# Kernel optimization log

Measured on AMD Instinct MI355X. Metric: run time of the kernel, lower is better.

Reference implementation:

```python
import jax, jax.numpy as jnp
import numpy as np

N = 100000
E = 3200000
T = 8
F = 64


def _temporal_conv(x, src, dst, time_index, W, b):
    # time-bucketed segmented scatter-add: segment id = dst*T + t
    seg = dst * T + time_index                      # [E]
    msgs = x[src]                                   # [E, F] gather (x_j)
    agg = jax.ops.segment_sum(msgs, seg, num_segments=N * T)  # [N*T, F]
    cat = agg.reshape(N, T * x.shape[-1])           # concat over t blocks: [N, T*F]
    return jax.nn.relu(cat @ W + b)                 # temporal_lin + relu


def setup_inputs() -> dict:
    key = jax.random.key(0)
    ks = jax.random.split(key, 10)
    x = jax.random.normal(ks[0], (N, F), dtype=jnp.float32)
    edge_index = jax.random.randint(ks[1], (2, E), 0, N, dtype=jnp.int64)
    time_index = jax.random.randint(ks[2], (E,), 0, T, dtype=jnp.int64)
    s1 = 1.0 / np.sqrt(F * T)
    W1 = jax.random.uniform(ks[3], (F * T, 64), jnp.float32, -s1, s1)
    b1 = jax.random.uniform(ks[4], (64,), jnp.float32, -s1, s1)
    s2 = 1.0 / np.sqrt(64 * T)
    W2 = jax.random.uniform(ks[5], (64 * T, 64), jnp.float32, -s2, s2)
    b2 = jax.random.uniform(ks[6], (64,), jnp.float32, -s2, s2)
    s3 = 1.0 / np.sqrt(64)
    Wssl = jax.random.uniform(ks[7], (64, F), jnp.float32, -s3, s3)
    bssl = jax.random.uniform(ks[8], (F,), jnp.float32, -s3, s3)
    return {"x": x, "edge_index": edge_index, "time_index": time_index,
            "W1": W1, "b1": b1, "W2": W2, "b2": b2, "Wssl": Wssl, "bssl": bssl}


def reference(x, edge_index, time_index, W1, b1, W2, b2, Wssl, bssl):
    src, dst = edge_index[0], edge_index[1]  # flow source_to_target
    h = _temporal_conv(x, src, dst, time_index, W1, b1)
    h = jax.nn.relu(h)                        # outer relu in TemporalSSTGNN.forward
    h = _temporal_conv(h, src, dst, time_index, W2, b2)
    ssl = h @ Wssl + bssl                     # self_supervised_linear
    return (h, ssl)
```

## Files before the change

kernel.cpp:

```cpp
#include <hip/hip_runtime.h>
#include <hip/hip_bf16.h>

#define N_NODES 100000
#define N_EDGES 3200000
#define NB 391
#define NBP 400
#define CAP 9216
#define PCAP 20480
#define ZNODE N_NODES
#define AROW 520
#define HROW 72

typedef __attribute__((ext_vector_type(8))) short short8;
typedef __attribute__((ext_vector_type(4))) float floatx4;
typedef __attribute__((ext_vector_type(2))) float f32x2;

__device__ __forceinline__ unsigned short f2bf(float f) {
    unsigned int u = __builtin_bit_cast(unsigned int, f);
    unsigned int r = (u + 0x7FFFu + ((u >> 16) & 1u)) >> 16;
    return (unsigned short)r;
}

__global__ __launch_bounds__(1024) void k_bscatter(const int* __restrict__ ei,
                                                   const int* __restrict__ ti,
                                                   int* __restrict__ cursor,
                                                   unsigned int* __restrict__ words,
                                                   const float* __restrict__ x,
                                                   unsigned short* __restrict__ xb,
                                                   unsigned short* __restrict__ h1b,
                                                   const float* __restrict__ W1,
                                                   const float* __restrict__ W2,
                                                   const float* __restrict__ Wssl,
                                                   unsigned short* __restrict__ Wf1,
                                                   unsigned short* __restrict__ Wf2,
                                                   unsigned short* __restrict__ Wsf) {
    __shared__ int h[NBP];
    __shared__ int bb[NBP];
    int tid = threadIdx.x;
    if (tid < NBP) h[tid] = 0;
    __syncthreads();
    int base = blockIdx.x * 4096;
    int breg[4], ofs[4];
    unsigned wreg[4];
#pragma unroll
    for (int i = 0; i < 4; ++i) {
        int e = base + i * 1024 + tid;
        bool v = e < N_EDGES;
        int dst = v ? ei[N_EDGES + e] : 0;
        int src = v ? ei[e] : 0;
        int tt  = v ? ti[e] : 0;
        int b = dst >> 8;
        breg[i] = v ? b : -1;
        wreg[i] = ((unsigned)src << 11) | ((unsigned)(dst & 255) << 3) | (unsigned)tt;
        ofs[i] = v ? atomicAdd(&h[b], 1) : 0;
    }
    __syncthreads();
    if (tid < NB) {
        int c = h[tid];
        bb[tid] = c ? atomicAdd(&cursor[tid], c) : 0;
    }
    __syncthreads();
#pragma unroll
    for (int i = 0; i < 4; ++i)
        if (breg[i] >= 0) {
            int b = breg[i];
            words[b * CAP + bb[b] + ofs[i]] = wreg[i];
        }

    int gtid = blockIdx.x * 1024 + tid;
    size_t xo = (size_t)gtid * 8;
    if (xo < (size_t)N_NODES * 64) {
        float4 f0 = *(const float4*)(x + xo);
        float4 f1 = *(const float4*)(x + xo + 4);
        unsigned r0, r1, r2, r3;
        asm("v_cvt_pk_bf16_f32 %0, %1, %2" : "=v"(r0) : "v"(f0.x), "v"(f0.y));
        asm("v_cvt_pk_bf16_f32 %0, %1, %2" : "=v"(r1) : "v"(f0.z), "v"(f0.w));
        asm("v_cvt_pk_bf16_f32 %0, %1, %2" : "=v"(r2) : "v"(f1.x), "v"(f1.y));
        asm("v_cvt_pk_bf16_f32 %0, %1, %2" : "=v"(r3) : "v"(f1.z), "v"(f1.w));
        uint4 st; st.x = r0; st.y = r1; st.z = r2; st.w = r3;
        *(uint4*)(xb + xo) = st;
    }
    if (gtid < 64) {
        xb[(size_t)ZNODE * 64 + gtid] = 0;
        h1b[(size_t)ZNODE * 64 + gtid] = 0;
    }
    if (gtid < 512 * 64) {
        int k = gtid >> 6, o = gtid & 63;
        int c = o >> 4, m = o & 15;
        int ks = k >> 5, q = (k >> 3) & 3, j = k & 7;
        int pos = (((c * 16 + ks) * 64) + (m + 16 * q)) * 8 + j;
        Wf1[pos] = f2bf(W1[gtid]);
        Wf2[pos] = f2bf(W2[gtid]);
    }
    if (gtid < 64 * 64) {
        int k = gtid >> 6, o = gtid & 63;
        int c = o >> 4, m = o & 15;
        int ks = k >> 5, q = (k >> 3) & 3, j = k & 7;
        int pos = (((c * 2 + ks) * 64) + (m + 16 * q)) * 8 + j;
        Wsf[pos] = f2bf(Wssl[gtid]);
    }
}

__global__ __launch_bounds__(1024) void k_lsort(const int* __restrict__ cursor,
                                                const unsigned int* __restrict__ words,
                                                int2* __restrict__ node_pm,
                                                int* __restrict__ gid_pad) {
    __shared__ int h[2048];
    __shared__ int nb[256];
    __shared__ int s_ml[256];
    __shared__ int wsum[4];
    int tid = threadIdx.x;
    int b = blockIdx.x;
    int rb = b * CAP, re = rb + cursor[b];
    h[tid] = 0; h[tid + 1024] = 0;
    __syncthreads();
    unsigned wreg[9];
    int ofs[9];
#pragma unroll
    for (int i = 0; i < 9; ++i) {
        int e = rb + i * 1024 + tid;
        bool v = e < re;
        unsigned w = v ? words[e] : 0u;
        wreg[i] = w;
        ofs[i] = v ? atomicAdd(&h[w & 2047u], 1) : -1;
    }
    __syncthreads();
    int sz = 0;
    if (tid < 256) {
        int m = 0;
#pragma unroll
        for (int t = 0; t < 8; ++t) { int c = h[tid * 8 + t]; m = c > m ? c : m; }
        m = (m + 3) & ~3;
        if (m < 8) m = 8;
        s_ml[tid] = m;
        sz = m * 8;
    }
    int lane = tid & 63, wv = tid >> 6;
    int inc = sz;
#pragma unroll
    for (int off = 1; off < 64; off <<= 1) {
        int t = __shfl_up(inc, off, 64);
        if (lane >= off) inc += t;
    }
    if (tid < 256 && lane == 63) wsum[wv] = inc;
    __syncthreads();
    int bsz = wsum[0] + wsum[1] + wsum[2] + wsum[3];
    if (tid < 256) {
        int basec = 0;
        for (int w = 0; w < wv; ++w) basec += wsum[w];
        nb[tid] = basec + inc - sz;
    }
    int pbase = b * PCAP;
    for (int s = tid; s < bsz; s += 1024) gid_pad[pbase + s] = ZNODE;
    int gn = b * 256 + tid;
    if (tid < 256 && gn < N_NODES) node_pm[gn] = (int2){pbase + nb[tid], s_ml[tid]};
    __syncthreads();
#pragma unroll
    for (int i = 0; i < 9; ++i)
        if (ofs[i] >= 0) {
            unsigned w = wreg[i];
            int ls = (int)(w & 2047u);
            int nd = ls >> 3, t = ls & 7;
            gid_pad[pbase + nb[nd] + t * s_ml[nd] + ofs[i]] = (int)(w >> 11);
        }
}


__device__ __forceinline__ void accumP(f32x2* a, uint4 p) {
    uint2 u;
    u.x = p.x << 16; u.y = p.x & 0xFFFF0000u;
    a[0] += __builtin_bit_cast(f32x2, u);
    u.x = p.y << 16; u.y = p.y & 0xFFFF0000u;
    a[1] += __builtin_bit_cast(f32x2, u);
    u.x = p.z << 16; u.y = p.z & 0xFFFF0000u;
    a[2] += __builtin_bit_cast(f32x2, u);
    u.x = p.w << 16; u.y = p.w & 0xFFFF0000u;
    a[3] += __builtin_bit_cast(f32x2, u);
}

__global__ __launch_bounds__(512) void k_fused(const int2* __restrict__ node_pm,
                                               const int* __restrict__ gid_pad,
                                               const unsigned short* __restrict__ xb,
                                               const unsigned short* __restrict__ Wf,
                                               const float* __restrict__ bias,
                                               const unsigned short* __restrict__ Wsf,
                                               const float* __restrict__ bssl,
                                               unsigned short* __restrict__ out_bf,
                                               float* __restrict__ out_f32,
                                               float* __restrict__ ssl_out) {
    __shared__ __align__(16) unsigned short Atile[32 * AROW];
    int tid = threadIdx.x;
    int wave = tid >> 6, lane = tid & 63;
    int node_base = blockIdx.x * 32;
    int tl = lane >> 3, fo = lane & 7;
    const uint4* xs = (const uint4*)xb;

    int2 pm[4];
#pragma unroll
    for (int i = 0; i < 4; ++i) pm[i] = node_pm[node_base + wave * 4 + i];

    int pb[4], ml[4];
    const int* gp[4];
#pragma unroll
    for (int i = 0; i < 4; ++i) {
        pb[i] = __builtin_amdgcn_readfirstlane(pm[i].x);
        ml[i] = __builtin_amdgcn_readfirstlane(pm[i].y);
        gp[i] = gid_pad + pb[i] + tl * ml[i];
    }
    int4 ga[4], gb[4];
#pragma unroll
    for (int i = 0; i < 4; ++i) {
        ga[i] = *(const int4*)(gp[i]);
        gb[i] = *(const int4*)(gp[i] + 4);
    }

#pragma unroll
    for (int pr = 0; pr < 2; ++pr) {
        int i0 = pr * 2, i1 = i0 + 1;
        uint4 p0 = xs[((unsigned)ga[i0].x << 3) + fo];
        uint4 p1 = xs[((unsigned)ga[i0].y << 3) + fo];
        uint4 p2 = xs[((unsigned)ga[i0].z << 3) + fo];
        uint4 p3 = xs[((unsigned)ga[i0].w << 3) + fo];
        uint4 p4 = xs[((unsigned)gb[i0].x << 3) + fo];
        uint4 p5 = xs[((unsigned)gb[i0].y << 3) + fo];
        uint4 p6 = xs[((unsigned)gb[i0].z << 3) + fo];
        uint4 p7 = xs[((unsigned)gb[i0].w << 3) + fo];
        uint4 q0 = xs[((unsigned)ga[i1].x << 3) + fo];
        uint4 q1 = xs[((unsigned)ga[i1].y << 3) + fo];
        uint4 q2 = xs[((unsigned)ga[i1].z << 3) + fo];
        uint4 q3 = xs[((unsigned)ga[i1].w << 3) + fo];
        uint4 q4 = xs[((unsigned)gb[i1].x << 3) + fo];
        uint4 q5 = xs[((unsigned)gb[i1].y << 3) + fo];
        uint4 q6 = xs[((unsigned)gb[i1].z << 3) + fo];
        uint4 q7 = xs[((unsigned)gb[i1].w << 3) + fo];
        f32x2 a0[4] = {{0.f,0.f},{0.f,0.f},{0.f,0.f},{0.f,0.f}};
        f32x2 a1[4] = {{0.f,0.f},{0.f,0.f},{0.f,0.f},{0.f,0.f}};
        accumP(a0, p0); accumP(a0, p1); accumP(a0, p2); accumP(a0, p3);
        accumP(a0, p4); accumP(a0, p5); accumP(a0, p6); accumP(a0, p7);
        accumP(a1, q0); accumP(a1, q1); accumP(a1, q2); accumP(a1, q3);
        accumP(a1, q4); accumP(a1, q5); accumP(a1, q6); accumP(a1, q7);
#pragma unroll 1
        for (int k = 8; k < ml[i0]; k += 4) {
            int4 g = *(const int4*)(gp[i0] + k);
            uint4 t0 = xs[((unsigned)g.x << 3) + fo];
            uint4 t1 = xs[((unsigned)g.y << 3) + fo];
            uint4 t2 = xs[((unsigned)g.z << 3) + fo];
            uint4 t3 = xs[((unsigned)g.w << 3) + fo];
            accumP(a0, t0); accumP(a0, t1); accumP(a0, t2); accumP(a0, t3);
        }
#pragma unroll 1
        for (int k = 8; k < ml[i1]; k += 4) {
            int4 g = *(const int4*)(gp[i1] + k);
            uint4 t0 = xs[((unsigned)g.x << 3) + fo];
            uint4 t1 = xs[((unsigned)g.y << 3) + fo];
            uint4 t2 = xs[((unsigned)g.z << 3) + fo];
            uint4 t3 = xs[((unsigned)g.w << 3) + fo];
            accumP(a1, t0); accumP(a1, t1); accumP(a1, t2); accumP(a1, t3);
        }
        unsigned r0, r1, r2, r3;
        asm("v_cvt_pk_bf16_f32 %0, %1, %2" : "=v"(r0) : "v"(a0[0].x), "v"(a0[0].y));
        asm("v_cvt_pk_bf16_f32 %0, %1, %2" : "=v"(r1) : "v"(a0[1].x), "v"(a0[1].y));
        asm("v_cvt_pk_bf16_f32 %0, %1, %2" : "=v"(r2) : "v"(a0[2].x), "v"(a0[2].y));
        asm("v_cvt_pk_bf16_f32 %0, %1, %2" : "=v"(r3) : "v"(a0[3].x), "v"(a0[3].y));
        uint4 st; st.x = r0; st.y = r1; st.z = r2; st.w = r3;
        *(uint4*)(&Atile[(wave * 4 + i0) * AROW + tl * 64 + fo * 8]) = st;
        asm("v_cvt_pk_bf16_f32 %0, %1, %2" : "=v"(r0) : "v"(a1[0].x), "v"(a1[0].y));
        asm("v_cvt_pk_bf16_f32 %0, %1, %2" : "=v"(r1) : "v"(a1[1].x), "v"(a1[1].y));
        asm("v_cvt_pk_bf16_f32 %0, %1, %2" : "=v"(r2) : "v"(a1[2].x), "v"(a1[2].y));
        asm("v_cvt_pk_bf16_f32 %0, %1, %2" : "=v"(r3) : "v"(a1[3].x), "v"(a1[3].y));
        st.x = r0; st.y = r1; st.z = r2; st.w = r3;
        *(uint4*)(&Atile[(wave * 4 + i1) * AROW + tl * 64 + fo * 8]) = st;
    }
    __syncthreads();

    int nt = wave >> 2, c = wave & 3;
    int m = lane & 15, q = lane >> 4;
    floatx4 acc = (floatx4){0.f, 0.f, 0.f, 0.f};
    const short8* wf8 = (const short8*)Wf;
    const unsigned short* abase = &Atile[(nt * 16 + m) * AROW + q * 8];
#pragma unroll
    for (int ks = 0; ks < 16; ++ks) {
        short8 a = *(const short8*)(abase + ks * 32);
        short8 b = wf8[(c * 16 + ks) * 64 + lane];
        acc = __builtin_amdgcn_mfma_f32_16x16x32_bf16(a, b, acc, 0, 0, 0);
    }
    float bb = bias[c * 16 + m];
    int node0 = node_base + nt * 16;
    float vv[4];
#pragma unroll
    for (int i = 0; i < 4; ++i) {
        float v = acc[i] + bb;
        vv[i] = v > 0.f ? v : 0.f;
        int node = node0 + q * 4 + i;
        size_t idx = (size_t)node * 64 + c * 16 + m;
        if (out_bf)  out_bf[idx] = f2bf(vv[i]);
        if (out_f32) out_f32[idx] = vv[i];
    }

    if (ssl_out) {
        __syncthreads();
        unsigned short* Ht = Atile;
#pragma unroll
        for (int i = 0; i < 4; ++i) {
            int nl = nt * 16 + q * 4 + i;
            Ht[nl * HROW + c * 16 + m] = f2bf(vv[i]);
        }
        __syncthreads();
        int nt2 = wave >> 2, c2 = wave & 3;
        floatx4 sacc = (floatx4){0.f, 0.f, 0.f, 0.f};
        const short8* sw8 = (const short8*)Wsf;
        const unsigned short* sab = &Ht[(nt2 * 16 + m) * HROW + q * 8];
#pragma unroll
        for (int ks = 0; ks < 2; ++ks) {
            short8 a = *(const short8*)(sab + ks * 32);
            short8 b = sw8[(c2 * 2 + ks) * 64 + lane];
            sacc = __builtin_amdgcn_mfma_f32_16x16x32_bf16(a, b, sacc, 0, 0, 0);
        }
        float sb = bssl[c2 * 16 + m];
        int n0 = node_base + nt2 * 16;
#pragma unroll
        for (int i = 0; i < 4; ++i) {
            int node = n0 + q * 4 + i;
            ssl_out[(size_t)node * 64 + c2 * 16 + m] = sacc[i] + sb;
        }
    }
}


extern "C" void kernel_launch(void* const* d_in, const int* in_sizes, int n_in,
                              void* d_out, int out_size, void* d_ws, size_t ws_size,
                              hipStream_t stream) {
    const float* x    = (const float*)d_in[0];
    const int*   ei   = (const int*)d_in[1];
    const int*   ti   = (const int*)d_in[2];
    const float* W1   = (const float*)d_in[3];
    const float* b1   = (const float*)d_in[4];
    const float* W2   = (const float*)d_in[5];
    const float* b2   = (const float*)d_in[6];
    const float* Wssl = (const float*)d_in[7];
    const float* bssl = (const float*)d_in[8];
    float* out = (float*)d_out;

    char* w = (char*)d_ws;
    auto alloc = [&](size_t bytes) -> char* {
        char* p = w;
        w += (bytes + 255) & ~(size_t)255;
        return p;
    };
    int* cursor   = (int*)alloc((size_t)NBP * 4);
    unsigned int* words = (unsigned int*)alloc((size_t)NB * CAP * 4);
    int2* node_pm = (int2*)alloc((size_t)N_NODES * 8);
    int* gid_pad  = (int*)alloc((size_t)NB * PCAP * 4);
    unsigned short* xb  = (unsigned short*)alloc((size_t)(N_NODES + 1) * 64 * 2);
    unsigned short* h1b = (unsigned short*)alloc((size_t)(N_NODES + 1) * 64 * 2);
    unsigned short* Wf1 = (unsigned short*)alloc((size_t)512 * 64 * 2);
    unsigned short* Wf2 = (unsigned short*)alloc((size_t)512 * 64 * 2);
    unsigned short* Wsf = (unsigned short*)alloc((size_t)64 * 64 * 2);

    hipMemsetAsync(cursor, 0, (size_t)NBP * 4, stream);
    k_bscatter<<<(N_EDGES + 4095) / 4096, 1024, 0, stream>>>(ei, ti, cursor, words,
                                                             x, xb, h1b, W1, W2, Wssl,
                                                             Wf1, Wf2, Wsf);
    k_lsort<<<NB, 1024, 0, stream>>>(cursor, words, node_pm, gid_pad);

    k_fused<<<N_NODES / 32, 512, 0, stream>>>(node_pm, gid_pad, xb, Wf1, b1,
                                              nullptr, nullptr, h1b, nullptr, nullptr);
    k_fused<<<N_NODES / 32, 512, 0, stream>>>(node_pm, gid_pad, h1b, Wf2, b2,
                                              Wsf, bssl, nullptr, out,
                                              out + (size_t)N_NODES * 64);
}
```

Before: 303.1 us.

## Replace bucket-scatter plus local sort with global histogram, scan, and atomic fill

Edges are no longer binned into 256-node buckets and locally sorted in shared memory. A global per-(node,time) segment histogram is built with global atomics, a per-block scan turns counts into padded slot offsets, and a second pass over the edges atomically claims slots to write source ids. This removes the intermediate words buffer and the shared-memory local sort. In exchange it reads the edge arrays twice, issues 6.4M global atomics spread over 800K counters, and adds a kernel launch.

```diff
diff --git a/kernel.cpp b/kernel.cpp
--- a/kernel.cpp
+++ b/kernel.cpp
@@ -4,9 +4,8 @@
 #define N_NODES 100000
 #define N_EDGES 3200000
 #define NB 391
-#define NBP 400
-#define CAP 9216
 #define PCAP 20480
+#define NSEG 800000
 #define ZNODE N_NODES
 #define AROW 520
 #define HROW 72
@@ -21,51 +20,32 @@
     return (unsigned short)r;
 }
 
-__global__ __launch_bounds__(1024) void k_bscatter(const int* __restrict__ ei,
-                                                   const int* __restrict__ ti,
-                                                   int* __restrict__ cursor,
-                                                   unsigned int* __restrict__ words,
-                                                   const float* __restrict__ x,
-                                                   unsigned short* __restrict__ xb,
-                                                   unsigned short* __restrict__ h1b,
-                                                   const float* __restrict__ W1,
-                                                   const float* __restrict__ W2,
-                                                   const float* __restrict__ Wssl,
-                                                   unsigned short* __restrict__ Wf1,
-                                                   unsigned short* __restrict__ Wf2,
-                                                   unsigned short* __restrict__ Wsf) {
-    __shared__ int h[NBP];
-    __shared__ int bb[NBP];
+__global__ __launch_bounds__(1024) void k_hist(const int* __restrict__ ei,
+                                               const int* __restrict__ ti,
+                                               int* __restrict__ segp,
+                                               const float* __restrict__ x,
+                                               unsigned short* __restrict__ xb,
+                                               unsigned short* __restrict__ h1b,
+                                               const float* __restrict__ W1,
+                                               const float* __restrict__ W2,
+                                               const float* __restrict__ Wssl,
+                                               unsigned short* __restrict__ Wf1,
+                                               unsigned short* __restrict__ Wf2,
+                                               unsigned short* __restrict__ Wsf) {
     int tid = threadIdx.x;
-    if (tid < NBP) h[tid] = 0;
-    __syncthreads();
     int base = blockIdx.x * 4096;
-    int breg[4], ofs[4];
-    unsigned wreg[4];
+    int seg[4]; bool v[4];
 #pragma unroll
     for (int i = 0; i < 4; ++i) {
         int e = base + i * 1024 + tid;
-        bool v = e < N_EDGES;
-        int dst = v ? ei[N_EDGES + e] : 0;
-        int src = v ? ei[e] : 0;
-        int tt  = v ? ti[e] : 0;
-        int b = dst >> 8;
-        breg[i] = v ? b : -1;
-        wreg[i] = ((unsigned)src << 11) | ((unsigned)(dst & 255) << 3) | (unsigned)tt;
-        ofs[i] = v ? atomicAdd(&h[b], 1) : 0;
-    }
-    __syncthreads();
-    if (tid < NB) {
-        int c = h[tid];
-        bb[tid] = c ? atomicAdd(&cursor[tid], c) : 0;
-    }
-    __syncthreads();
+        v[i] = e < N_EDGES;
+        int dst = v[i] ? ei[N_EDGES + e] : 0;
+        int tt  = v[i] ? ti[e] : 0;
+        seg[i] = dst * 8 + tt;
+    }
 #pragma unroll
     for (int i = 0; i < 4; ++i)
-        if (breg[i] >= 0) {
-            int b = breg[i];
-            words[b * CAP + bb[b] + ofs[i]] = wreg[i];
-        }
+        if (v[i]) atomicAdd(&segp[seg[i]], 1);
 
     int gtid = blockIdx.x * 1024 + tid;
     size_t xo = (size_t)gtid * 8;
@@ -101,40 +81,29 @@
     }
 }
 
-__global__ __launch_bounds__(1024) void k_lsort(const int* __restrict__ cursor,
-                                                const unsigned int* __restrict__ words,
-                                                int2* __restrict__ node_pm,
-                                                int* __restrict__ gid_pad) {
-    __shared__ int h[2048];
-    __shared__ int nb[256];
-    __shared__ int s_ml[256];
+__global__ __launch_bounds__(256) void k_scan(int* __restrict__ segp,
+                                              int2* __restrict__ node_pm,
+                                              int* __restrict__ gid_pad) {
     __shared__ int wsum[4];
     int tid = threadIdx.x;
     int b = blockIdx.x;
-    int rb = b * CAP, re = rb + cursor[b];
-    h[tid] = 0; h[tid + 1024] = 0;
-    __syncthreads();
-    unsigned wreg[9];
-    int ofs[9];
-#pragma unroll
-    for (int i = 0; i < 9; ++i) {
-        int e = rb + i * 1024 + tid;
-        bool v = e < re;
-        unsigned w = v ? words[e] : 0u;
-        wreg[i] = w;
-        ofs[i] = v ? atomicAdd(&h[w & 2047u], 1) : -1;
-    }
-    __syncthreads();
-    int sz = 0;
-    if (tid < 256) {
-        int m = 0;
-#pragma unroll
-        for (int t = 0; t < 8; ++t) { int c = h[tid * 8 + t]; m = c > m ? c : m; }
-        m = (m + 3) & ~3;
-        if (m < 8) m = 8;
-        s_ml[tid] = m;
-        sz = m * 8;
-    }
+    int gn = b * 256 + tid;
+    bool valid = gn < N_NODES;
+    int4 c0 = {0, 0, 0, 0}, c1 = {0, 0, 0, 0};
+    if (valid) {
+        c0 = *(const int4*)(segp + (size_t)gn * 8);
+        c1 = *(const int4*)(segp + (size_t)gn * 8 + 4);
+    }
+    int m01 = c0.x > c0.y ? c0.x : c0.y;
+    int m23 = c0.z > c0.w ? c0.z : c0.w;
+    int m45 = c1.x > c1.y ? c1.x : c1.y;
+    int m67 = c1.z > c1.w ? c1.z : c1.w;
+    int m = m01 > m23 ? m01 : m23;
+    int m2 = m45 > m67 ? m45 : m67;
+    m = m > m2 ? m : m2;
+    m = (m + 3) & ~3;
+    if (m < 8) m = 8;
+    int sz = valid ? m * 8 : 0;
     int lane = tid & 63, wv = tid >> 6;
     int inc = sz;
 #pragma unroll
@@ -142,26 +111,47 @@
         int t = __shfl_up(inc, off, 64);
         if (lane >= off) inc += t;
     }
-    if (tid < 256 && lane == 63) wsum[wv] = inc;
+    if (lane == 63) wsum[wv] = inc;
     __syncthreads();
+    int basec = 0;
+    for (int w = 0; w < wv; ++w) basec += wsum[w];
+    int nb = basec + inc - sz;
     int bsz = wsum[0] + wsum[1] + wsum[2] + wsum[3];
-    if (tid < 256) {
-        int basec = 0;
-        for (int w = 0; w < wv; ++w) basec += wsum[w];
-        nb[tid] = basec + inc - sz;
-    }
     int pbase = b * PCAP;
-    for (int s = tid; s < bsz; s += 1024) gid_pad[pbase + s] = ZNODE;
-    int gn = b * 256 + tid;
-    if (tid < 256 && gn < N_NODES) node_pm[gn] = (int2){pbase + nb[tid], s_ml[tid]};
-    __syncthreads();
-#pragma unroll
-    for (int i = 0; i < 9; ++i)
-        if (ofs[i] >= 0) {
-            unsigned w = wreg[i];
-            int ls = (int)(w & 2047u);
-            int nd = ls >> 3, t = ls & 7;
-            gid_pad[pbase + nb[nd] + t * s_ml[nd] + ofs[i]] = (int)(w >> 11);
+    if (valid) {
+        node_pm[gn] = (int2){pbase + nb, m};
+        int p = pbase + nb;
+        int4 s0 = {p, p + m, p + 2 * m, p + 3 * m};
+        int4 s1 = {p + 4 * m, p + 5 * m, p + 6 * m, p + 7 * m};
+        *(int4*)(segp + (size_t)gn * 8) = s0;
+        *(int4*)(segp + (size_t)gn * 8 + 4) = s1;
+    }
+    int4 z = {ZNODE, ZNODE, ZNODE, ZNODE};
+    for (int s = tid * 4; s < bsz; s += 1024)
+        *(int4*)(gid_pad + pbase + s) = z;
+}
+
+__global__ __launch_bounds__(1024) void k_fill(const int* __restrict__ ei,
+                                               const int* __restrict__ ti,
+                                               int* __restrict__ segp,
+                                               int* __restrict__ gid_pad) {
+    int tid = threadIdx.x;
+    int base = blockIdx.x * 4096;
+    int src[4], seg[4]; bool v[4];
+#pragma unroll
+    for (int i = 0; i < 4; ++i) {
+        int e = base + i * 1024 + tid;
+        v[i] = e < N_EDGES;
+        src[i] = v[i] ? ei[e] : 0;
+        int dst = v[i] ? ei[N_EDGES + e] : 0;
+        int tt  = v[i] ? ti[e] : 0;
+        seg[i] = dst * 8 + tt;
+    }
+#pragma unroll
+    for (int i = 0; i < 4; ++i)
+        if (v[i]) {
+            int pos = atomicAdd(&segp[seg[i]], 1);
+            gid_pad[pos] = src[i];
         }
 }
 
@@ -347,8 +337,7 @@
         w += (bytes + 255) & ~(size_t)255;
         return p;
     };
-    int* cursor   = (int*)alloc((size_t)NBP * 4);
-    unsigned int* words = (unsigned int*)alloc((size_t)NB * CAP * 4);
+    int* segp     = (int*)alloc((size_t)NSEG * 4);
     int2* node_pm = (int2*)alloc((size_t)N_NODES * 8);
     int* gid_pad  = (int*)alloc((size_t)NB * PCAP * 4);
     unsigned short* xb  = (unsigned short*)alloc((size_t)(N_NODES + 1) * 64 * 2);
@@ -357,11 +346,12 @@
     unsigned short* Wf2 = (unsigned short*)alloc((size_t)512 * 64 * 2);
     unsigned short* Wsf = (unsigned short*)alloc((size_t)64 * 64 * 2);
 
-    hipMemsetAsync(cursor, 0, (size_t)NBP * 4, stream);
-    k_bscatter<<<(N_EDGES + 4095) / 4096, 1024, 0, stream>>>(ei, ti, cursor, words,
-                                                             x, xb, h1b, W1, W2, Wssl,
-                                                             Wf1, Wf2, Wsf);
-    k_lsort<<<NB, 1024, 0, stream>>>(cursor, words, node_pm, gid_pad);
+    hipMemsetAsync(segp, 0, (size_t)NSEG * 4, stream);
+    k_hist<<<(N_EDGES + 4095) / 4096, 1024, 0, stream>>>(ei, ti, segp,
+                                                         x, xb, h1b, W1, W2, Wssl,
+                                                         Wf1, Wf2, Wsf);
+    k_scan<<<NB, 256, 0, stream>>>(segp, node_pm, gid_pad);
+    k_fill<<<(N_EDGES + 4095) / 4096, 1024, 0, stream>>>(ei, ti, segp, gid_pad);
 
     k_fused<<<N_NODES / 32, 512, 0, stream>>>(node_pm, gid_pad, xb, Wf1, b1,
                                               nullptr, nullptr, h1b, nullptr, nullptr);
```

Result: slower. 660.9 us (+118.1%).
